# Performance work log

Measured on AMD Instinct MI355X. Metric: run time of the kernel, lower is better.

Reference implementation:

```python
import jax, jax.numpy as jnp
import numpy as np

N_NODES = 50000
N_EDGES = 600000
LATENT = 128
STEPS = 4
BN_EPS = 1e-5


def _bn(h, gamma, beta):
    # BatchNorm1d in training mode: batch statistics over the row dim (biased var)
    mean = jnp.mean(h, axis=0)
    var = jnp.var(h, axis=0)
    return gamma * (h - mean) * jax.lax.rsqrt(var + BN_EPS) + beta


def setup_inputs() -> dict:
    key = jax.random.key(0)
    ks = jax.random.split(key, 9)
    L, S = LATENT, STEPS
    d = {}
    d["x"] = jax.random.normal(ks[0], (N_NODES, L), dtype=jnp.float32)
    d["edge_attr"] = jax.random.normal(ks[1], (N_EDGES, L), dtype=jnp.float32)
    d["edge_index"] = jax.random.randint(ks[2], (2, N_EDGES), 0, N_NODES, dtype=jnp.int64)
    # MLP weights: small init (BN normalizes hidden activations anyway)
    d["edge_W1"] = jax.random.normal(ks[3], (S, 3 * L, L), dtype=jnp.float32) * (1.0 / np.sqrt(3 * L))
    d["edge_b1"] = jnp.zeros((S, L), jnp.float32)
    d["edge_g1"] = jnp.ones((S, L), jnp.float32)
    d["edge_be1"] = jnp.zeros((S, L), jnp.float32)
    d["edge_W2"] = jax.random.normal(ks[4], (S, L, L), dtype=jnp.float32) * (1.0 / np.sqrt(L))
    d["edge_b2"] = jnp.zeros((S, L), jnp.float32)
    d["node_W1"] = jax.random.normal(ks[5], (S, 2 * L, L), dtype=jnp.float32) * (1.0 / np.sqrt(2 * L))
    d["node_b1"] = jnp.zeros((S, L), jnp.float32)
    d["node_g1"] = jnp.ones((S, L), jnp.float32)
    d["node_be1"] = jnp.zeros((S, L), jnp.float32)
    d["node_W2"] = jax.random.normal(ks[6], (S, L, L), dtype=jnp.float32) * (1.0 / np.sqrt(L))
    d["node_b2"] = jnp.zeros((S, L), jnp.float32)
    return d


def reference(x, edge_attr, edge_index, edge_W1, edge_b1, edge_g1, edge_be1,
              edge_W2, edge_b2, node_W1, node_b1, node_g1, node_be1,
              node_W2, node_b2):
    src = edge_index[0]  # x_j (source)
    dst = edge_index[1]  # x_i (target), also the scatter target
    for s in range(STEPS):
        # --- edge update (message) ---
        m = jnp.concatenate([x[dst], x[src], edge_attr], axis=1)  # [E, 3L]
        h = _bn(m @ edge_W1[s] + edge_b1[s], edge_g1[s], edge_be1[s])
        h = jax.nn.relu(h)
        h = jax.nn.relu(h @ edge_W2[s] + edge_b2[s])
        edge_attr = h + edge_attr  # residual
        # --- aggregate: scatter-sum to target nodes ---
        agg = jax.ops.segment_sum(edge_attr, dst, num_segments=N_NODES)  # [N, L]
        # --- node update ---
        n = jnp.concatenate([x, agg], axis=1)  # [N, 2L]
        h = _bn(n @ node_W1[s] + node_b1[s], node_g1[s], node_be1[s])
        h = jax.nn.relu(h)
        h = jax.nn.relu(h @ node_W2[s] + node_b2[s])
        x = h + x  # residual
    return x, edge_attr
```

## Files before the change

kernel.cpp:

```cpp
#include <hip/hip_runtime.h>
#include <hip/hip_bf16.h>
#include <cstdint>
#include <cstddef>

#define E_N 600000
#define NND 50000
#define L 128

typedef unsigned short u16;
typedef unsigned int u32;
typedef __attribute__((ext_vector_type(8))) short bf16x8;
typedef __attribute__((ext_vector_type(4))) float f32x4;

static __device__ __forceinline__ u16 f2bf(float f) {
  union { float f; u32 u; } c; c.f = f;
  return (u16)((c.u + 0x7fffu + ((c.u >> 16) & 1u)) >> 16);
}
static __device__ __forceinline__ u32 pk2(float a, float b) {
  return (u32)f2bf(a) | ((u32)f2bf(b) << 16);
}
static __device__ __forceinline__ float bf2f(u32 h) {
  union { u32 u; float f; } c; c.u = (h & 0xffffu) << 16; return c.f;
}
static __device__ __forceinline__ void atomAddF(float* p, float v) {
#if defined(__HIP_DEVICE_COMPILE__)
  unsafeAtomicAdd(p, v);
#else
  atomicAdd(p, v);
#endif
}
static __device__ __forceinline__ bf16x8 bnrelu8(bf16x8 raw, float4 sca, float4 scb,
                                                 float4 sha, float4 shb) {
  union { bf16x8 v; u16 h[8]; } in; in.v = raw;
  const float sc[8] = {sca.x, sca.y, sca.z, sca.w, scb.x, scb.y, scb.z, scb.w};
  const float sh[8] = {sha.x, sha.y, sha.z, sha.w, shb.x, shb.y, shb.z, shb.w};
  float f[8];
  #pragma unroll
  for (int i = 0; i < 8; ++i) f[i] = fmaxf(bf2f(in.h[i]) * sc[i] + sh[i], 0.f);
  union { bf16x8 v; u32 w[4]; } r;
  #pragma unroll
  for (int i = 0; i < 4; ++i) r.w[i] = pk2(f[2 * i], f[2 * i + 1]);
  return r.v;
}

#define MFMA(a, bfr, c) __builtin_amdgcn_mfma_f32_16x16x32_bf16((a), (bfr), (c), 0, 0, 0)

__global__ __launch_bounds__(256) void k_cvt4(const float* __restrict__ in,
                                              u16* __restrict__ out, int n4) {
  const int i = blockIdx.x * 256 + threadIdx.x;
  if (i < n4) {
    const float4 v = *(const float4*)(in + (size_t)i * 4);
    uint2 o; o.x = pk2(v.x, v.y); o.y = pk2(v.z, v.w);
    *(uint2*)(out + (size_t)i * 4) = o;
  }
}

__global__ void k_wt(const float* __restrict__ W, u16* __restrict__ Wt, int K) {
  const int idx = blockIdx.x * 256 + threadIdx.x;
  const int total = 4 * K * 128;
  if (idx >= total) return;
  const int s = idx / (K * 128);
  const int rem = idx - s * K * 128;
  const int n = rem / K;
  const int k = rem - n * K;
  Wt[idx] = f2bf(W[(size_t)s * K * 128 + (size_t)k * 128 + n]);
}

__global__ void k_hist(const int* __restrict__ dstI, int* __restrict__ cnt) {
  const int i = blockIdx.x * 256 + threadIdx.x;
  if (i < E_N) atomicAdd(&cnt[dstI[i]], 1);
}

__global__ __launch_bounds__(1024) void k_scan(const int* __restrict__ cnt, int* __restrict__ startA) {
  __shared__ int buf[1024];
  __shared__ int carry;
  const int tid = threadIdx.x;
  if (tid == 0) carry = 0;
  __syncthreads();
  for (int base = 0; base < NND; base += 1024) {
    int v = (base + tid < NND) ? cnt[base + tid] : 0;
    buf[tid] = v;
    __syncthreads();
    for (int off = 1; off < 1024; off <<= 1) {
      int t = (tid >= off) ? buf[tid - off] : 0;
      __syncthreads();
      buf[tid] += t;
      __syncthreads();
    }
    const int incl = buf[tid];
    const int c = carry;
    if (base + tid < NND) startA[base + tid] = c + incl - v;
    __syncthreads();
    if (tid == 1023) carry = c + incl;
    __syncthreads();
  }
  if (tid == 0) startA[NND] = carry;
}

__global__ void k_fill(const int* __restrict__ dstI, const int* __restrict__ startA,
                       int* __restrict__ cur, int* __restrict__ eids) {
  const int i = blockIdx.x * 256 + threadIdx.x;
  if (i < E_N) {
    const int d = dstI[i];
    const int pos = atomicAdd(&cur[d], 1);
    eids[startA[d] + pos] = i;
  }
}

__global__ void k_perm(const int* __restrict__ srcI, const int* __restrict__ dstI,
                       const int* __restrict__ perm,
                       int* __restrict__ srcP, int* __restrict__ dstP) {
  const int i = blockIdx.x * 256 + threadIdx.x;
  if (i < E_N) {
    const int e = perm[i];
    srcP[i] = srcI[e];
    dstP[i] = dstI[e];
  }
}

__global__ __launch_bounds__(256) void k_agg(const u16* __restrict__ ea16,
                                             const int* __restrict__ startA,
                                             u16* __restrict__ agg16) {
  const int node = blockIdx.x * 4 + (threadIdx.x >> 6);
  const int lane = threadIdx.x & 63;
  if (node >= NND) return;
  const int s = startA[node], e = startA[node + 1];
  float a0 = 0.f, a1 = 0.f, b0 = 0.f, b1 = 0.f;
  int i = s;
  for (; i + 1 < e; i += 2) {
    const u32 v0 = *(const u32*)(ea16 + (size_t)i * L + lane * 2);
    const u32 v1 = *(const u32*)(ea16 + (size_t)(i + 1) * L + lane * 2);
    a0 += bf2f(v0); a1 += bf2f(v0 >> 16);
    b0 += bf2f(v1); b1 += bf2f(v1 >> 16);
  }
  if (i < e) {
    const u32 v = *(const u32*)(ea16 + (size_t)i * L + lane * 2);
    a0 += bf2f(v); a1 += bf2f(v >> 16);
  }
  *(u32*)(agg16 + (size_t)node * L + lane * 2) = pk2(a0 + b0, a1 + b1);
}

__global__ void k_bnfin(const float* __restrict__ gS, const float* __restrict__ g,
                        const float* __restrict__ be, float invM, float* __restrict__ ss) {
  const int c = threadIdx.x;
  float s1 = 0.f, s2 = 0.f;
  for (int j = 0; j < 64; ++j) { s1 += gS[j * L + c]; s2 += gS[64 * L + j * L + c]; }
  const float mean = s1 * invM;
  const float var = s2 * invM - mean * mean;
  const float sc = g[c] * rsqrtf(var + 1e-5f);
  ss[c] = sc;
  ss[L + c] = be[c] - mean * sc;
}

template <bool EA32>
__global__ __launch_bounds__(512, 3) void k_edge_l1(
    const u16* __restrict__ x16, const float* __restrict__ ea32,
    const u16* __restrict__ ea16, const int* __restrict__ perm,
    const int* __restrict__ srcP, const int* __restrict__ dstP,
    const u16* __restrict__ Wt, const float* __restrict__ b,
    u16* __restrict__ h1, float* __restrict__ gS)
{
  __shared__ __align__(16) char AsB[3 * 16384];
  __shared__ float red[256];
  const int tid = threadIdx.x, bid = blockIdx.x, row0 = bid * 128;
  const int lane = tid & 63, wid = tid >> 6;
  const int l15 = lane & 15, lq = lane >> 4;
  const int col = wid * 16 + l15;

  const int kcMap[6] = {4, 5, 0, 1, 2, 3};
  bf16x8 Bf[12];
  #pragma unroll
  for (int cc = 0; cc < 6; ++cc)
    #pragma unroll
    for (int k2 = 0; k2 < 2; ++k2)
      Bf[cc * 2 + k2] = *(const bf16x8*)(Wt + (size_t)col * 384 + kcMap[cc] * 64 + k2 * 32 + lq * 8);

  const int srow = tid >> 2, spart = tid & 3;
  const int crow = min(row0 + srow, E_N - 1);
  const int sd = dstP[crow], ssr = srcP[crow];
  const int prow = EA32 ? perm[crow] : 0;

  f32x4 acc[8];
  #pragma unroll
  for (int m = 0; m < 8; ++m) acc[m] = (f32x4){0.f, 0.f, 0.f, 0.f};

  uint4 ra[2], rb[2];
  auto sload = [&](int cc, uint4* v) {
    if (cc >= 2) {
      const int node = (cc >= 4) ? ssr : sd;
      const u16* p = x16 + (size_t)node * L + (cc & 1) * 64 + spart * 16;
      v[0] = *(const uint4*)p; v[1] = *(const uint4*)(p + 8);
    } else if (EA32) {
      const float* p = ea32 + (size_t)prow * L + cc * 64 + spart * 16;
      const float4 f0 = *(const float4*)p,       f1 = *(const float4*)(p + 4);
      const float4 f2 = *(const float4*)(p + 8), f3 = *(const float4*)(p + 12);
      v[0].x = pk2(f0.x, f0.y); v[0].y = pk2(f0.z, f0.w);
      v[0].z = pk2(f1.x, f1.y); v[0].w = pk2(f1.z, f1.w);
      v[1].x = pk2(f2.x, f2.y); v[1].y = pk2(f2.z, f2.w);
      v[1].z = pk2(f3.x, f3.y); v[1].w = pk2(f3.z, f3.w);
    } else {
      const u16* p = ea16 + (size_t)crow * L + cc * 64 + spart * 16;
      v[0] = *(const uint4*)p; v[1] = *(const uint4*)(p + 8);
    }
  };
  auto swrite = [&](int buf, const uint4* v) {
    char* base = AsB + buf * 16384;
    const int sw = (srow & 7) << 4;
    const int b0 = srow * 128 + spart * 32;
    *(uint4*)(base + (b0 ^ sw)) = v[0];
    *(uint4*)(base + ((b0 + 16) ^ sw)) = v[1];
  };

  sload(0, ra); sload(1, rb);
  swrite(0, ra);
  __syncthreads();
  #pragma unroll
  for (int cc = 0; cc < 6; ++cc) {
    if (cc + 2 < 6) sload(cc + 2, (cc & 1) ? rb : ra);
    if (cc + 1 < 6) swrite((cc + 1) % 3, (cc & 1) ? ra : rb);
    const char* base = AsB + (cc % 3) * 16384;
    #pragma unroll
    for (int m = 0; m < 8; ++m) {
      const int row = m * 16 + l15;
      const int sw = (row & 7) << 4;
      #pragma unroll
      for (int k2 = 0; k2 < 2; ++k2) {
        const bf16x8 af = *(const bf16x8*)(base + ((row * 128 + k2 * 64 + lq * 16) ^ sw));
        acc[m] = MFMA(Bf[cc * 2 + k2], af, acc[m]);
      }
    }
    __syncthreads();
  }

  const int colb = wid * 16 + lq * 4;
  float bb[4];
  #pragma unroll
  for (int r = 0; r < 4; ++r) bb[r] = b[colb + r];
  float s1[4] = {0.f, 0.f, 0.f, 0.f}, s2[4] = {0.f, 0.f, 0.f, 0.f};
  #pragma unroll
  for (int m = 0; m < 8; ++m) {
    const int row = row0 + m * 16 + l15;
    if (row < E_N) {
      ushort4 st;
      float o0 = acc[m][0] + bb[0], o1 = acc[m][1] + bb[1];
      float o2 = acc[m][2] + bb[2], o3 = acc[m][3] + bb[3];
      s1[0] += o0; s2[0] += o0 * o0; s1[1] += o1; s2[1] += o1 * o1;
      s1[2] += o2; s2[2] += o2 * o2; s1[3] += o3; s2[3] += o3 * o3;
      st.x = f2bf(o0); st.y = f2bf(o1); st.z = f2bf(o2); st.w = f2bf(o3);
      *(ushort4*)(h1 + (size_t)row * L + colb) = st;
    }
  }
  #pragma unroll
  for (int off = 1; off < 16; off <<= 1) {
    #pragma unroll
    for (int r = 0; r < 4; ++r) {
      s1[r] += __shfl_xor(s1[r], off);
      s2[r] += __shfl_xor(s2[r], off);
    }
  }
  if (l15 == 0) {
    float4 v1; v1.x = s1[0]; v1.y = s1[1]; v1.z = s1[2]; v1.w = s1[3];
    float4 v2; v2.x = s2[0]; v2.y = s2[1]; v2.z = s2[2]; v2.w = s2[3];
    *(float4*)(&red[colb]) = v1;
    *(float4*)(&red[128 + colb]) = v2;
  }
  __syncthreads();
  const int slot = (bid & 63) * L;
  if (tid < 128) atomAddF(&gS[slot + tid], red[tid]);
  else if (tid < 256) atomAddF(&gS[64 * L + slot + (tid - 128)], red[tid]);
}

template <bool EA32, bool WF32>
__global__ __launch_bounds__(512, 4) void k_edge_l2(
    const u16* __restrict__ h1, const float* __restrict__ ss,
    const u16* __restrict__ Wt, const float* __restrict__ b,
    const float* __restrict__ resid32, const u16* __restrict__ resid16,
    const int* __restrict__ perm,
    float* __restrict__ ea_out, u16* __restrict__ ea16)
{
  __shared__ __align__(16) char AsB[2 * 16384];
  const int tid = threadIdx.x, bid = blockIdx.x, row0 = bid * 128;
  const int lane = tid & 63, wid = tid >> 6;
  const int l15 = lane & 15, lq = lane >> 4;
  const int col = wid * 16 + l15;

  bf16x8 Bf[4];
  #pragma unroll
  for (int k = 0; k < 4; ++k)
    Bf[k] = *(const bf16x8*)(Wt + (size_t)col * 128 + k * 32 + lq * 8);

  const int srow = tid >> 2, spart = tid & 3;
  const int crow = min(row0 + srow, E_N - 1);

  #pragma unroll
  for (int cc = 0; cc < 2; ++cc) {
    const int kb = cc * 64 + spart * 16;
    const float4 c0 = *(const float4*)(ss + kb),      c1 = *(const float4*)(ss + kb + 4);
    const float4 c2 = *(const float4*)(ss + kb + 8),  c3 = *(const float4*)(ss + kb + 12);
    const float4 g0 = *(const float4*)(ss + 128 + kb),     g1 = *(const float4*)(ss + 128 + kb + 4);
    const float4 g2 = *(const float4*)(ss + 128 + kb + 8), g3 = *(const float4*)(ss + 128 + kb + 12);
    const u16* p = h1 + (size_t)crow * L + kb;
    bf16x8 r0 = *(const bf16x8*)p, r1 = *(const bf16x8*)(p + 8);
    r0 = bnrelu8(r0, c0, c1, g0, g1);
    r1 = bnrelu8(r1, c2, c3, g2, g3);
    char* base = AsB + cc * 16384;
    const int sw = (srow & 7) << 4;
    const int b0 = srow * 128 + spart * 32;
    *(bf16x8*)(base + (b0 ^ sw)) = r0;
    *(bf16x8*)(base + ((b0 + 16) ^ sw)) = r1;
  }
  __syncthreads();

  f32x4 acc[8];
  #pragma unroll
  for (int m = 0; m < 8; ++m) acc[m] = (f32x4){0.f, 0.f, 0.f, 0.f};
  #pragma unroll
  for (int cc = 0; cc < 2; ++cc) {
    const char* base = AsB + cc * 16384;
    #pragma unroll
    for (int m = 0; m < 8; ++m) {
      const int row = m * 16 + l15;
      const int sw = (row & 7) << 4;
      #pragma unroll
      for (int k2 = 0; k2 < 2; ++k2) {
        const bf16x8 af = *(const bf16x8*)(base + ((row * 128 + k2 * 64 + lq * 16) ^ sw));
        acc[m] = MFMA(Bf[cc * 2 + k2], af, acc[m]);
      }
    }
  }

  const int colb = wid * 16 + lq * 4;
  float bb[4];
  #pragma unroll
  for (int r = 0; r < 4; ++r) bb[r] = b[colb + r];
  #pragma unroll
  for (int m = 0; m < 8; ++m) {
    const int row = row0 + m * 16 + l15;
    if (row < E_N) {
      float o[4];
      #pragma unroll
      for (int r = 0; r < 4; ++r) o[r] = fmaxf(acc[m][r] + bb[r], 0.f);
      if (EA32) {
        const float4 rv = *(const float4*)(resid32 + (size_t)perm[row] * L + colb);
        o[0] += rv.x; o[1] += rv.y; o[2] += rv.z; o[3] += rv.w;
      } else {
        const ushort4 rv = *(const ushort4*)(resid16 + (size_t)row * L + colb);
        o[0] += bf2f(rv.x); o[1] += bf2f(rv.y); o[2] += bf2f(rv.z); o[3] += bf2f(rv.w);
      }
      ushort4 st;
      st.x = f2bf(o[0]); st.y = f2bf(o[1]); st.z = f2bf(o[2]); st.w = f2bf(o[3]);
      *(ushort4*)(ea16 + (size_t)row * L + colb) = st;
      if (WF32) {
        float4 fv; fv.x = o[0]; fv.y = o[1]; fv.z = o[2]; fv.w = o[3];
        *(float4*)(ea_out + (size_t)perm[row] * L + colb) = fv;
      }
    }
  }
}

__global__ __launch_bounds__(256) void k_node_l1(
    const u16* __restrict__ x16, const u16* __restrict__ agg16,
    const u16* __restrict__ Wt, const float* __restrict__ b,
    u16* __restrict__ h1, float* __restrict__ gS)
{
  __shared__ __align__(16) char Bs[2][16384];
  __shared__ float red[256];
  const int tid = threadIdx.x, bid = blockIdx.x, row0 = bid * 64;
  red[tid] = 0.f;
  const int lane = tid & 63, wid = tid >> 6, wr = wid >> 1, wc = wid & 1;
  const int l15 = lane & 15, lq = lane >> 4;
  const int r0 = row0 + wr * 32 + l15, r1 = r0 + 16;
  const int rr0 = min(r0, NND - 1), rr1 = min(r1, NND - 1);

  const u16* aP[2][2];
  aP[0][0] = x16 + (size_t)rr0 * L;   aP[1][0] = x16 + (size_t)rr1 * L;
  aP[0][1] = agg16 + (size_t)rr0 * L; aP[1][1] = agg16 + (size_t)rr1 * L;

  f32x4 acc[2][4];
  #pragma unroll
  for (int m = 0; m < 2; ++m)
    #pragma unroll
    for (int n = 0; n < 4; ++n) acc[m][n] = (f32x4){0.f, 0.f, 0.f, 0.f};

  auto loadA = [&](int c, bf16x8 (&af)[2][2]) {
    const int seg = c >> 1;
    const int base = (c & 1) * 64 + lq * 8;
    #pragma unroll
    for (int k2 = 0; k2 < 2; ++k2) {
      af[0][k2] = *(const bf16x8*)(aP[0][seg] + base + k2 * 32);
      af[1][k2] = *(const bf16x8*)(aP[1][seg] + base + k2 * 32);
    }
  };
  auto stage = [&](int c, int buf) {
    #pragma unroll
    for (int i = 0; i < 4; ++i) {
      const int slot = tid + i * 256;
      const int n = slot >> 3, kq = slot & 7;
      const uint4 v = *(const uint4*)(Wt + (size_t)n * 256 + c * 64 + kq * 8);
      *(uint4*)(&Bs[buf][0] + ((n * 128 + kq * 16) ^ ((n & 7) << 4))) = v;
    }
  };

  bf16x8 aCur[2][2], aNxt[2][2];
  loadA(0, aCur);
  stage(0, 0);
  __syncthreads();
  #pragma unroll
  for (int c = 0; c < 4; ++c) {
    if (c + 1 < 4) loadA(c + 1, aNxt);
    {
      const char* base = &Bs[c & 1][0];
      #pragma unroll
      for (int k2 = 0; k2 < 2; ++k2)
        #pragma unroll
        for (int n = 0; n < 4; ++n) {
          const int ncol = wc * 64 + n * 16 + l15;
          const bf16x8 bfr = *(const bf16x8*)(base + ((ncol * 128 + k2 * 64 + lq * 16) ^ ((ncol & 7) << 4)));
          acc[0][n] = MFMA(aCur[0][k2], bfr, acc[0][n]);
          acc[1][n] = MFMA(aCur[1][k2], bfr, acc[1][n]);
        }
    }
    if (c + 1 < 4) stage(c + 1, (c + 1) & 1);
    __syncthreads();
    #pragma unroll
    for (int m = 0; m < 2; ++m)
      #pragma unroll
      for (int k2 = 0; k2 < 2; ++k2) aCur[m][k2] = aNxt[m][k2];
  }

  float bb[4], s1[4], s2[4];
  #pragma unroll
  for (int n = 0; n < 4; ++n) { bb[n] = b[wc * 64 + n * 16 + l15]; s1[n] = 0.f; s2[n] = 0.f; }
  #pragma unroll
  for (int m = 0; m < 2; ++m)
    #pragma unroll
    for (int n = 0; n < 4; ++n) {
      const int ncol = wc * 64 + n * 16 + l15;
      #pragma unroll
      for (int r = 0; r < 4; ++r) {
        const int row = row0 + wr * 32 + m * 16 + lq * 4 + r;
        if (row < NND) {
          const float o = acc[m][n][r] + bb[n];
          s1[n] += o; s2[n] += o * o;
          h1[(size_t)row * L + ncol] = f2bf(o);
        }
      }
    }
  #pragma unroll
  for (int n = 0; n < 4; ++n) {
    const int ncol = wc * 64 + n * 16 + l15;
    atomAddF(&red[ncol], s1[n]);
    atomAddF(&red[128 + ncol], s2[n]);
  }
  __syncthreads();
  const int slot = (bid & 63) * L;
  if (tid < 128) atomAddF(&gS[slot + tid], red[tid]);
  else atomAddF(&gS[64 * L + slot + (tid - 128)], red[tid]);
}

__global__ __launch_bounds__(256) void k_node_l2(
    const u16* __restrict__ h1, const float* __restrict__ ss,
    const u16* __restrict__ Wt, const float* __restrict__ b,
    const float* __restrict__ resid, float* __restrict__ x_out,
    u16* __restrict__ x16)
{
  __shared__ __align__(16) char Bs[2][16384];
  const int tid = threadIdx.x, bid = blockIdx.x, row0 = bid * 64;
  const int lane = tid & 63, wid = tid >> 6, wr = wid >> 1, wc = wid & 1;
  const int l15 = lane & 15, lq = lane >> 4;
  const int r0 = row0 + wr * 32 + l15, r1 = r0 + 16;
  const int rr0 = min(r0, NND - 1), rr1 = min(r1, NND - 1);
  const u16* a0 = h1 + (size_t)rr0 * L + lq * 8;
  const u16* a1 = h1 + (size_t)rr1 * L + lq * 8;

  f32x4 acc[2][4];
  #pragma unroll
  for (int m = 0; m < 2; ++m)
    #pragma unroll
    for (int n = 0; n < 4; ++n) acc[m][n] = (f32x4){0.f, 0.f, 0.f, 0.f};

  auto stage = [&](int c, int buf) {
    #pragma unroll
    for (int i = 0; i < 4; ++i) {
      const int slot = tid + i * 256;
      const int n = slot >> 3, kq = slot & 7;
      const uint4 v = *(const uint4*)(Wt + (size_t)n * 128 + c * 64 + kq * 8);
      *(uint4*)(&Bs[buf][0] + ((n * 128 + kq * 16) ^ ((n & 7) << 4))) = v;
    }
  };
  stage(0, 0);
  stage(1, 1);
  bf16x8 raw[2][2][2];
  #pragma unroll
  for (int c = 0; c < 2; ++c)
    #pragma unroll
    for (int k2 = 0; k2 < 2; ++k2) {
      raw[c][0][k2] = *(const bf16x8*)(a0 + c * 64 + k2 * 32);
      raw[c][1][k2] = *(const bf16x8*)(a1 + c * 64 + k2 * 32);
    }
  __syncthreads();

  #pragma unroll
  for (int c = 0; c < 2; ++c) {
    bf16x8 af[2][2];
    #pragma unroll
    for (int k2 = 0; k2 < 2; ++k2) {
      const int kg = c * 64 + k2 * 32 + lq * 8;
      const float4 sca = *(const float4*)(ss + kg), scb = *(const float4*)(ss + kg + 4);
      const float4 sha = *(const float4*)(ss + 128 + kg), shb = *(const float4*)(ss + 128 + kg + 4);
      af[0][k2] = bnrelu8(raw[c][0][k2], sca, scb, sha, shb);
      af[1][k2] = bnrelu8(raw[c][1][k2], sca, scb, sha, shb);
    }
    const char* base = &Bs[c][0];
    #pragma unroll
    for (int k2 = 0; k2 < 2; ++k2)
      #pragma unroll
      for (int n = 0; n < 4; ++n) {
        const int ncol = wc * 64 + n * 16 + l15;
        const bf16x8 bfr = *(const bf16x8*)(base + ((ncol * 128 + k2 * 64 + lq * 16) ^ ((ncol & 7) << 4)));
        acc[0][n] = MFMA(af[0][k2], bfr, acc[0][n]);
        acc[1][n] = MFMA(af[1][k2], bfr, acc[1][n]);
      }
  }

  float bb[4];
  #pragma unroll
  for (int n = 0; n < 4; ++n) bb[n] = b[wc * 64 + n * 16 + l15];
  #pragma unroll
  for (int m = 0; m < 2; ++m)
    #pragma unroll
    for (int n = 0; n < 4; ++n) {
      const int ncol = wc * 64 + n * 16 + l15;
      #pragma unroll
      for (int r = 0; r < 4; ++r) {
        const int row = row0 + wr * 32 + m * 16 + lq * 4 + r;
        if (row < NND) {
          const float o = fmaxf(acc[m][n][r] + bb[n], 0.f) + resid[(size_t)row * L + ncol];
          x_out[(size_t)row * L + ncol] = o;
          x16[(size_t)row * L + ncol] = f2bf(o);
        }
      }
    }
}

extern "C" void kernel_launch(void* const* d_in, const int* in_sizes, int n_in,
                              void* d_out, int out_size, void* d_ws, size_t ws_size,
                              hipStream_t stream) {
  (void)in_sizes; (void)n_in; (void)out_size; (void)ws_size;
  const float* in_x  = (const float*)d_in[0];
  const float* in_ea = (const float*)d_in[1];
  const int*   ei    = (const int*)d_in[2];
  const float* eW1 = (const float*)d_in[3];
  const float* eb1 = (const float*)d_in[4];
  const float* eg1 = (const float*)d_in[5];
  const float* ebe1= (const float*)d_in[6];
  const float* eW2 = (const float*)d_in[7];
  const float* eb2 = (const float*)d_in[8];
  const float* nW1 = (const float*)d_in[9];
  const float* nb1 = (const float*)d_in[10];
  const float* ng1 = (const float*)d_in[11];
  const float* nbe1= (const float*)d_in[12];
  const float* nW2 = (const float*)d_in[13];
  const float* nb2 = (const float*)d_in[14];

  float* x  = (float*)d_out;
  float* ea = (float*)d_out + (size_t)NND * L;

  char* w = (char*)d_ws;
  u16* h1e   = (u16*)w;   w += (size_t)E_N * L * sizeof(u16);
  u16* ea16  = (u16*)w;   w += (size_t)E_N * L * sizeof(u16);
  u16* h1n   = (u16*)w;   w += (size_t)NND * L * sizeof(u16);
  u16* x16   = (u16*)w;   w += (size_t)NND * L * sizeof(u16);
  u16* agg16 = (u16*)w;   w += (size_t)NND * L * sizeof(u16);
  float* gS  = (float*)w; w += (size_t)2 * 64 * L * sizeof(float);
  float* ss  = (float*)w; w += 4096;
  u16* eW1t = (u16*)w;   w += (size_t)4 * 128 * 384 * sizeof(u16);
  u16* eW2t = (u16*)w;   w += (size_t)4 * 128 * 128 * sizeof(u16);
  u16* nW1t = (u16*)w;   w += (size_t)4 * 128 * 256 * sizeof(u16);
  u16* nW2t = (u16*)w;   w += (size_t)4 * 128 * 128 * sizeof(u16);
  int* cnt    = (int*)w; w += (size_t)NND * sizeof(int);
  int* cur    = (int*)w; w += (size_t)NND * sizeof(int);
  int* startA = (int*)w; w += (size_t)(NND + 64) * sizeof(int);
  int* eids   = (int*)w; w += (size_t)E_N * sizeof(int);
  int* srcP   = (int*)w; w += (size_t)E_N * sizeof(int);
  int* dstP   = (int*)w; w += (size_t)E_N * sizeof(int);

  const int* srcI = ei;
  const int* dstI = ei + E_N;

  k_cvt4<<<(NND * L / 4 + 255) / 256, 256, 0, stream>>>(in_x, x16, NND * L / 4);
  k_wt<<<(4 * 384 * 128 + 255) / 256, 256, 0, stream>>>(eW1, eW1t, 384);
  k_wt<<<(4 * 128 * 128 + 255) / 256, 256, 0, stream>>>(eW2, eW2t, 128);
  k_wt<<<(4 * 256 * 128 + 255) / 256, 256, 0, stream>>>(nW1, nW1t, 256);
  k_wt<<<(4 * 128 * 128 + 255) / 256, 256, 0, stream>>>(nW2, nW2t, 128);
  hipMemsetAsync(cnt, 0, (size_t)NND * sizeof(int), stream);
  hipMemsetAsync(cur, 0, (size_t)NND * sizeof(int), stream);
  k_hist<<<(E_N + 255) / 256, 256, 0, stream>>>(dstI, cnt);
  k_scan<<<1, 1024, 0, stream>>>(cnt, startA);
  k_fill<<<(E_N + 255) / 256, 256, 0, stream>>>(dstI, startA, cur, eids);
  k_perm<<<(E_N + 255) / 256, 256, 0, stream>>>(srcI, dstI, eids, srcP, dstP);

  const int egrid = (E_N + 127) / 128;
  const int ngrid = (NND + 63) / 64;

  for (int s = 0; s < 4; ++s) {
    hipMemsetAsync(gS, 0, (size_t)2 * 64 * L * sizeof(float), stream);
    if (s == 0)
      k_edge_l1<true><<<egrid, 512, 0, stream>>>(x16, in_ea, nullptr, eids, srcP, dstP,
          eW1t + (size_t)s * 128 * 384, eb1 + (size_t)s * L, h1e, gS);
    else
      k_edge_l1<false><<<egrid, 512, 0, stream>>>(x16, nullptr, ea16, eids, srcP, dstP,
          eW1t + (size_t)s * 128 * 384, eb1 + (size_t)s * L, h1e, gS);
    k_bnfin<<<1, 128, 0, stream>>>(gS, eg1 + (size_t)s * L, ebe1 + (size_t)s * L,
        1.f / (float)E_N, ss);
    if (s == 0)
      k_edge_l2<true, false><<<egrid, 512, 0, stream>>>(h1e, ss,
          eW2t + (size_t)s * 128 * 128, eb2 + (size_t)s * L, in_ea, nullptr, eids, ea, ea16);
    else if (s < 3)
      k_edge_l2<false, false><<<egrid, 512, 0, stream>>>(h1e, ss,
          eW2t + (size_t)s * 128 * 128, eb2 + (size_t)s * L, nullptr, ea16, eids, ea, ea16);
    else
      k_edge_l2<false, true><<<egrid, 512, 0, stream>>>(h1e, ss,
          eW2t + (size_t)s * 128 * 128, eb2 + (size_t)s * L, nullptr, ea16, eids, ea, ea16);
    k_agg<<<(NND + 3) / 4, 256, 0, stream>>>(ea16, startA, agg16);
    hipMemsetAsync(gS, 0, (size_t)2 * 64 * L * sizeof(float), stream);
    k_node_l1<<<ngrid, 256, 0, stream>>>(x16, agg16,
        nW1t + (size_t)s * 128 * 256, nb1 + (size_t)s * L, h1n, gS);
    k_bnfin<<<1, 128, 0, stream>>>(gS, ng1 + (size_t)s * L, nbe1 + (size_t)s * L,
        1.f / (float)NND, ss);
    k_node_l2<<<ngrid, 256, 0, stream>>>(h1n, ss,
        nW2t + (size_t)s * 128 * 128, nb2 + (size_t)s * L,
        (s == 0) ? in_x : x, x, x16);
  }
}
```

Before: 2.212 ms.

## Store edge intermediates in panel-blocked layout for coalesced tile access

Changes the bf16 edge buffers (h1e and ea16) from row-major to a blocked layout. Each 128-row block is split into 8 column panels of 16 elements, stored contiguously. Every producer and consumer kernel (edge L1 and L2 load and store, residual read, and aggregation) is updated to the new addressing. The goal is contiguous per-wave stores and loads inside the MFMA tiles, where row-strided accesses were scattered before. The trade-off is that the aggregation kernel now reads 8 separate 32-byte chunks per edge row instead of one contiguous row.

```diff
diff --git a/kernel.cpp b/kernel.cpp
--- a/kernel.cpp
+++ b/kernel.cpp
@@ -6,6 +6,8 @@
 #define E_N 600000
 #define NND 50000
 #define L 128
+#define EGRID 4688
+#define PBLK 16384
 
 typedef unsigned short u16;
 typedef unsigned int u32;
@@ -44,6 +46,10 @@
 }
 
 #define MFMA(a, bfr, c) __builtin_amdgcn_mfma_f32_16x16x32_bf16((a), (bfr), (c), 0, 0, 0)
+
+static __device__ __forceinline__ size_t paddr(int row, int panel, int incol) {
+  return (size_t)(row >> 7) * PBLK + (size_t)panel * 2048 + (size_t)(row & 127) * 16 + incol;
+}
 
 __global__ __launch_bounds__(256) void k_cvt4(const float* __restrict__ in,
                                               u16* __restrict__ out, int n4) {
@@ -125,16 +131,18 @@
   const int lane = threadIdx.x & 63;
   if (node >= NND) return;
   const int s = startA[node], e = startA[node + 1];
+  const size_t poff = (size_t)(lane >> 3) * 2048 + (size_t)((lane & 7) * 2);
   float a0 = 0.f, a1 = 0.f, b0 = 0.f, b1 = 0.f;
   int i = s;
   for (; i + 1 < e; i += 2) {
-    const u32 v0 = *(const u32*)(ea16 + (size_t)i * L + lane * 2);
-    const u32 v1 = *(const u32*)(ea16 + (size_t)(i + 1) * L + lane * 2);
+    const u32 v0 = *(const u32*)(ea16 + (size_t)(i >> 7) * PBLK + (size_t)(i & 127) * 16 + poff);
+    const int j = i + 1;
+    const u32 v1 = *(const u32*)(ea16 + (size_t)(j >> 7) * PBLK + (size_t)(j & 127) * 16 + poff);
     a0 += bf2f(v0); a1 += bf2f(v0 >> 16);
     b0 += bf2f(v1); b1 += bf2f(v1 >> 16);
   }
   if (i < e) {
-    const u32 v = *(const u32*)(ea16 + (size_t)i * L + lane * 2);
+    const u32 v = *(const u32*)(ea16 + (size_t)(i >> 7) * PBLK + (size_t)(i & 127) * 16 + poff);
     a0 += bf2f(v); a1 += bf2f(v >> 16);
   }
   *(u32*)(agg16 + (size_t)node * L + lane * 2) = pk2(a0 + b0, a1 + b1);
@@ -199,7 +207,7 @@
       v[1].x = pk2(f2.x, f2.y); v[1].y = pk2(f2.z, f2.w);
       v[1].z = pk2(f3.x, f3.y); v[1].w = pk2(f3.z, f3.w);
     } else {
-      const u16* p = ea16 + (size_t)crow * L + cc * 64 + spart * 16;
+      const u16* p = ea16 + paddr(crow, cc * 4 + spart, 0);
       v[0] = *(const uint4*)p; v[1] = *(const uint4*)(p + 8);
     }
   };
@@ -237,17 +245,18 @@
   #pragma unroll
   for (int r = 0; r < 4; ++r) bb[r] = b[colb + r];
   float s1[4] = {0.f, 0.f, 0.f, 0.f}, s2[4] = {0.f, 0.f, 0.f, 0.f};
+  u16* hp = h1 + (size_t)bid * PBLK + (size_t)wid * 2048 + lq * 4;
   #pragma unroll
   for (int m = 0; m < 8; ++m) {
-    const int row = row0 + m * 16 + l15;
-    if (row < E_N) {
+    const int rl = m * 16 + l15;
+    if (row0 + rl < E_N) {
       ushort4 st;
       float o0 = acc[m][0] + bb[0], o1 = acc[m][1] + bb[1];
       float o2 = acc[m][2] + bb[2], o3 = acc[m][3] + bb[3];
       s1[0] += o0; s2[0] += o0 * o0; s1[1] += o1; s2[1] += o1 * o1;
       s1[2] += o2; s2[2] += o2 * o2; s1[3] += o3; s2[3] += o3 * o3;
       st.x = f2bf(o0); st.y = f2bf(o1); st.z = f2bf(o2); st.w = f2bf(o3);
-      *(ushort4*)(h1 + (size_t)row * L + colb) = st;
+      *(ushort4*)(hp + rl * 16) = st;
     }
   }
   #pragma unroll
@@ -299,7 +308,7 @@
     const float4 c2 = *(const float4*)(ss + kb + 8),  c3 = *(const float4*)(ss + kb + 12);
     const float4 g0 = *(const float4*)(ss + 128 + kb),     g1 = *(const float4*)(ss + 128 + kb + 4);
     const float4 g2 = *(const float4*)(ss + 128 + kb + 8), g3 = *(const float4*)(ss + 128 + kb + 12);
-    const u16* p = h1 + (size_t)crow * L + kb;
+    const u16* p = h1 + paddr(crow, cc * 4 + spart, 0);
     bf16x8 r0 = *(const bf16x8*)p, r1 = *(const bf16x8*)(p + 8);
     r0 = bnrelu8(r0, c0, c1, g0, g1);
     r1 = bnrelu8(r1, c2, c3, g2, g3);
@@ -333,9 +342,11 @@
   float bb[4];
   #pragma unroll
   for (int r = 0; r < 4; ++r) bb[r] = b[colb + r];
+  u16* ep = ea16 + (size_t)bid * PBLK + (size_t)wid * 2048 + lq * 4;
   #pragma unroll
   for (int m = 0; m < 8; ++m) {
-    const int row = row0 + m * 16 + l15;
+    const int rl = m * 16 + l15;
+    const int row = row0 + rl;
     if (row < E_N) {
       float o[4];
       #pragma unroll
@@ -344,12 +355,12 @@
         const float4 rv = *(const float4*)(resid32 + (size_t)perm[row] * L + colb);
         o[0] += rv.x; o[1] += rv.y; o[2] += rv.z; o[3] += rv.w;
       } else {
-        const ushort4 rv = *(const ushort4*)(resid16 + (size_t)row * L + colb);
+        const ushort4 rv = *(const ushort4*)(resid16 + (size_t)bid * PBLK + (size_t)wid * 2048 + rl * 16 + lq * 4);
         o[0] += bf2f(rv.x); o[1] += bf2f(rv.y); o[2] += bf2f(rv.z); o[3] += bf2f(rv.w);
       }
       ushort4 st;
       st.x = f2bf(o[0]); st.y = f2bf(o[1]); st.z = f2bf(o[2]); st.w = f2bf(o[3]);
-      *(ushort4*)(ea16 + (size_t)row * L + colb) = st;
+      *(ushort4*)(ep + rl * 16) = st;
       if (WF32) {
         float4 fv; fv.x = o[0]; fv.y = o[1]; fv.z = o[2]; fv.w = o[3];
         *(float4*)(ea_out + (size_t)perm[row] * L + colb) = fv;
@@ -567,8 +578,8 @@
   float* ea = (float*)d_out + (size_t)NND * L;
 
   char* w = (char*)d_ws;
-  u16* h1e   = (u16*)w;   w += (size_t)E_N * L * sizeof(u16);
-  u16* ea16  = (u16*)w;   w += (size_t)E_N * L * sizeof(u16);
+  u16* h1e   = (u16*)w;   w += (size_t)EGRID * PBLK * sizeof(u16);
+  u16* ea16  = (u16*)w;   w += (size_t)EGRID * PBLK * sizeof(u16);
   u16* h1n   = (u16*)w;   w += (size_t)NND * L * sizeof(u16);
   u16* x16   = (u16*)w;   w += (size_t)NND * L * sizeof(u16);
   u16* agg16 = (u16*)w;   w += (size_t)NND * L * sizeof(u16);
@@ -600,27 +611,26 @@
   k_fill<<<(E_N + 255) / 256, 256, 0, stream>>>(dstI, startA, cur, eids);
   k_perm<<<(E_N + 255) / 256, 256, 0, stream>>>(srcI, dstI, eids, srcP, dstP);
 
-  const int egrid = (E_N + 127) / 128;
   const int ngrid = (NND + 63) / 64;
 
   for (int s = 0; s < 4; ++s) {
     hipMemsetAsync(gS, 0, (size_t)2 * 64 * L * sizeof(float), stream);
     if (s == 0)
-      k_edge_l1<true><<<egrid, 512, 0, stream>>>(x16, in_ea, nullptr, eids, srcP, dstP,
+      k_edge_l1<true><<<EGRID, 512, 0, stream>>>(x16, in_ea, nullptr, eids, srcP, dstP,
           eW1t + (size_t)s * 128 * 384, eb1 + (size_t)s * L, h1e, gS);
     else
-      k_edge_l1<false><<<egrid, 512, 0, stream>>>(x16, nullptr, ea16, eids, srcP, dstP,
+      k_edge_l1<false><<<EGRID, 512, 0, stream>>>(x16, nullptr, ea16, eids, srcP, dstP,
           eW1t + (size_t)s * 128 * 384, eb1 + (size_t)s * L, h1e, gS);
     k_bnfin<<<1, 128, 0, stream>>>(gS, eg1 + (size_t)s * L, ebe1 + (size_t)s * L,
         1.f / (float)E_N, ss);
     if (s == 0)
-      k_edge_l2<true, false><<<egrid, 512, 0, stream>>>(h1e, ss,
+      k_edge_l2<true, false><<<EGRID, 512, 0, stream>>>(h1e, ss,
           eW2t + (size_t)s * 128 * 128, eb2 + (size_t)s * L, in_ea, nullptr, eids, ea, ea16);
     else if (s < 3)
-      k_edge_l2<false, false><<<egrid, 512, 0, stream>>>(h1e, ss,
+      k_edge_l2<false, false><<<EGRID, 512, 0, stream>>>(h1e, ss,
           eW2t + (size_t)s * 128 * 128, eb2 + (size_t)s * L, nullptr, ea16, eids, ea, ea16);
     else
-      k_edge_l2<false, true><<<egrid, 512, 0, stream>>>(h1e, ss,
+      k_edge_l2<false, true><<<EGRID, 512, 0, stream>>>(h1e, ss,
           eW2t + (size_t)s * 128 * 128, eb2 + (size_t)s * L, nullptr, ea16, eids, ea, ea16);
     k_agg<<<(NND + 3) / 4, 256, 0, stream>>>(ea16, startA, agg16);
     hipMemsetAsync(gS, 0, (size_t)2 * 64 * L * sizeof(float), stream);
```

Measured after the change: 2.183 ms. No clear change (-1.3%).
